# Kernel tuning notes

Measured on AMD Instinct MI355X. Metric: run time of the kernel, lower is better.

The kernel has to match this reference:

```python
import jax, jax.numpy as jnp
import numpy as np
from jax.ops import segment_sum

N = 100000
E = 2500000
F = 2
H = 32
L = 2


def setup_inputs() -> dict:
    key = jax.random.key(0)
    ks = jax.random.split(key, 12)
    s = 0.1
    node_features = jax.random.normal(ks[0], (N, F), dtype=jnp.float32)
    edge_index = jax.random.randint(ks[1], (2, E), 0, N, dtype=jnp.int64)
    W_in = jax.random.normal(ks[2], (F, H), dtype=jnp.float32) * s
    b_in = jnp.zeros((H,), dtype=jnp.float32)
    W_upd = jax.random.normal(ks[3], (L, 2 * H, H), dtype=jnp.float32) * s
    b_upd = jnp.zeros((L, H), dtype=jnp.float32)
    We1 = jax.random.normal(ks[4], (2 * H, H), dtype=jnp.float32) * s
    be1 = jnp.zeros((H,), dtype=jnp.float32)
    We2 = jax.random.normal(ks[5], (H, 1), dtype=jnp.float32) * s
    be2 = jnp.zeros((1,), dtype=jnp.float32)
    return {"node_features": node_features, "edge_index": edge_index,
            "W_in": W_in, "b_in": b_in, "W_upd": W_upd, "b_upd": b_upd,
            "We1": We1, "be1": be1, "We2": We2, "be2": be2}


def reference(node_features, edge_index, W_in, b_in, W_upd, b_upd, We1, be1, We2, be2):
    row, col = edge_index[0], edge_index[1]
    h = jax.nn.relu(node_features @ W_in + b_in)  # [N, H]
    # degree of each row node (bincount, clamped to >=1)
    deg = segment_sum(jnp.ones((E,), dtype=jnp.float32), row, num_segments=N)
    deg = jnp.maximum(deg, 1.0)[:, None]  # [N, 1]
    for l in range(L):
        agg = segment_sum(h[col], row, num_segments=N) / deg  # gather + scatter-add + normalize
        h = jax.nn.relu(jnp.concatenate([h, agg], axis=-1) @ W_upd[l] + b_upd[l])
    edge_feat = jnp.concatenate([h[row], h[col]], axis=-1)  # [E, 2H]
    hidden = jax.nn.relu(edge_feat @ We1 + be1)
    flux = (hidden @ We2 + be2)[:, 0]  # [E]
    return flux
```

## Files before the change

### kernel.cpp

```cpp
#include <hip/hip_runtime.h>
#include <hip/hip_fp16.h>

#define NN 100000
#define NE 2500000
#define RANGE 256
#define NBUCK 391
#define CHUNK 16384
#define NBLK_A ((NE + CHUNK - 1) / CHUNK)
#define BCAP 8192

__device__ __forceinline__ float relu_(float x){ return fmaxf(x, 0.f); }

__global__ __launch_bounds__(256) void k_node_embed16(
    const float* __restrict__ nf, const float* __restrict__ Win,
    const float* __restrict__ bin, __half* __restrict__ h16)
{
  int n = blockIdx.x * 256 + threadIdx.x;
  if (n >= NN) return;
  float f0 = nf[2*n], f1 = nf[2*n+1];
  const float4* W0 = (const float4*)Win;
  const float4* W1 = (const float4*)(Win + 32);
  const float4* B  = (const float4*)bin;
  __half2* g2 = (__half2*)(h16 + (size_t)n * 32);
#pragma unroll
  for (int j = 0; j < 8; ++j) {
    float4 w0 = W0[j], w1 = W1[j], b = B[j], r;
    r.x = relu_(fmaf(f0, w0.x, fmaf(f1, w1.x, b.x)));
    r.y = relu_(fmaf(f0, w0.y, fmaf(f1, w1.y, b.y)));
    r.z = relu_(fmaf(f0, w0.z, fmaf(f1, w1.z, b.z)));
    r.w = relu_(fmaf(f0, w0.w, fmaf(f1, w1.w, b.w)));
    g2[2*j]   = __floats2half2_rn(r.x, r.y);
    g2[2*j+1] = __floats2half2_rn(r.z, r.w);
  }
}


__global__ __launch_bounds__(512) void k_histA(const int* __restrict__ row,
                                               int* __restrict__ btot,
                                               int* __restrict__ blockhist)
{
  __shared__ int hist[NBUCK];
  int t = threadIdx.x;
  for (int i = t; i < NBUCK; i += 512) hist[i] = 0;
  __syncthreads();
  int e0 = blockIdx.x * CHUNK + t;
#pragma unroll
  for (int k = 0; k < CHUNK / 512; ++k) {
    int e = e0 + k * 512;
    if (e < NE) atomicAdd(&hist[row[e] >> 8], 1);
  }
  __syncthreads();
  for (int i = t; i < NBUCK; i += 512) {
    int c = hist[i];
    blockhist[(size_t)i * NBLK_A + blockIdx.x] = c;
    if (c) atomicAdd(&btot[i], c);
  }
}

__global__ __launch_bounds__(512) void k_scanA(const int* __restrict__ btot,
                                               int* __restrict__ bbase)
{
  __shared__ int s[512];
  int t = threadIdx.x;
  int my = (t < NBUCK) ? btot[t] : 0;
  s[t] = my;
  __syncthreads();
  for (int off = 1; off < 512; off <<= 1) {
    int v = (t >= off) ? s[t - off] : 0;
    __syncthreads();
    s[t] += v;
    __syncthreads();
  }
  if (t < NBUCK) bbase[t] = s[t] - my;
  if (t == 0) bbase[NBUCK] = NE;
}

__global__ __launch_bounds__(512) void k_colscan(int* __restrict__ blockhist,
                                                 const int* __restrict__ bbase)
{
  __shared__ int s[512];
  int i = blockIdx.x, t = threadIdx.x;
  int* rowp = blockhist + (size_t)i * NBLK_A;
  int my = (t < NBLK_A) ? rowp[t] : 0;
  s[t] = my;
  __syncthreads();
  for (int off = 1; off < 512; off <<= 1) {
    int v = (t >= off) ? s[t - off] : 0;
    __syncthreads();
    s[t] += v;
    __syncthreads();
  }
  if (t < NBLK_A) rowp[t] = bbase[i] + s[t] - my;
}

__global__ __launch_bounds__(512) void k_partition(
    const int* __restrict__ row, const int* __restrict__ col,
    const int* __restrict__ blockhist, unsigned int* __restrict__ keys)
{
  __shared__ int cur[NBUCK];
  __shared__ int base[NBUCK];
  int t = threadIdx.x, b = blockIdx.x;
  for (int i = t; i < NBUCK; i += 512) {
    base[i] = blockhist[(size_t)i * NBLK_A + b];
    cur[i] = 0;
  }
  __syncthreads();
  int e0 = b * CHUNK + t;
#pragma unroll
  for (int k = 0; k < CHUNK / 512; ++k) {
    int e = e0 + k * 512;
    if (e < NE) {
      int r = row[e];
      int bi = r >> 8;
      int idx = atomicAdd(&cur[bi], 1);
      keys[base[bi] + idx] = ((unsigned)col[e] << 8) | (unsigned)(r & 255);
    }
  }
}

__global__ __launch_bounds__(512) void k_passB_agg1(
    const int* __restrict__ bbase, const unsigned int* __restrict__ keys,
    const float* __restrict__ nf, const float* __restrict__ Win,
    const float* __restrict__ bin,
    int* __restrict__ ecol, int* __restrict__ rowptr,
    __half* __restrict__ agg16)
{
  __shared__ unsigned keysl[BCAP];
  __shared__ int hist[RANGE];
  __shared__ int sc[RANGE];
  __shared__ int segs[RANGE];
  __shared__ int sege[RANGE];
  int t = threadIdx.x, b = blockIdx.x;
  int s0 = bbase[b], e0 = bbase[b + 1];
  int cnt = e0 - s0;
  if (t < RANGE) hist[t] = 0;
  __syncthreads();
  for (int i = t; i < cnt; i += 512) {
    unsigned k = keys[s0 + i];
    if (i < BCAP) keysl[i] = k;
    atomicAdd(&hist[k & 255u], 1);
  }
  __syncthreads();
  int my = (t < RANGE) ? hist[t] : 0;
  if (t < RANGE) sc[t] = my;
  __syncthreads();
  for (int off = 1; off < RANGE; off <<= 1) {
    int v = 0;
    if (t < RANGE && t >= off) v = sc[t - off];
    __syncthreads();
    if (t < RANGE) sc[t] += v;
    __syncthreads();
  }
  if (t < RANGE) {
    int ex = sc[t] - my;
    int n = b * RANGE + t;
    if (n <= NN) rowptr[n] = s0 + ex;
    segs[t] = ex;
    sege[t] = sc[t];
    hist[t] = ex;
  }
  __syncthreads();
  for (int i = t; i < cnt; i += 512) {
    unsigned key = (i < BCAP) ? keysl[i] : keys[s0 + i];
    int rl = (int)(key & 255u);
    int idx = atomicAdd(&hist[rl], 1);
    ecol[s0 + idx] = (int)(key >> 8);
  }
  __syncthreads();

  const float2* nf2 = (const float2*)nf;
  for (int slot = t; slot < RANGE * 4; slot += 512) {
    int node = slot >> 2, q = slot & 3;
    int n = b * RANGE + node;
    if (n >= NN) continue;
    float w0[8], w1[8], bb[8];
#pragma unroll
    for (int j = 0; j < 8; ++j) {
      w0[j] = Win[q * 8 + j];
      w1[j] = Win[32 + q * 8 + j];
      bb[j] = bin[q * 8 + j];
    }
    int ss = segs[node], ee = sege[node];
    float acc[8];
#pragma unroll
    for (int j = 0; j < 8; ++j) acc[j] = 0.f;
    int i = ss;
    for (; i + 2 <= ee; i += 2) {
      int c0 = ecol[s0 + i], c1 = ecol[s0 + i + 1];
      float2 f0 = nf2[c0];
      float2 f1 = nf2[c1];
#pragma unroll
      for (int j = 0; j < 8; ++j) {
        acc[j] += relu_(fmaf(f0.x, w0[j], fmaf(f0.y, w1[j], bb[j])));
        acc[j] += relu_(fmaf(f1.x, w0[j], fmaf(f1.y, w1[j], bb[j])));
      }
    }
    if (i < ee) {
      float2 f = nf2[ecol[s0 + i]];
#pragma unroll
      for (int j = 0; j < 8; ++j)
        acc[j] += relu_(fmaf(f.x, w0[j], fmaf(f.y, w1[j], bb[j])));
    }
    float dinv = 1.0f / fmaxf((float)(ee - ss), 1.0f);
    uint4 pk;
    __half2* pp = (__half2*)&pk;
#pragma unroll
    for (int k = 0; k < 4; ++k)
      pp[k] = __floats2half2_rn(acc[2*k] * dinv, acc[2*k+1] * dinv);
    ((uint4*)agg16)[(size_t)n * 4 + q] = pk;
  }
}

__global__ __launch_bounds__(256) void k_update(
    const __half* __restrict__ h16in, const __half* __restrict__ agg16,
    const float* __restrict__ W, const float* __restrict__ b,
    __half* __restrict__ h16out)
{
  __shared__ float Ws[2048];
  __shared__ float bs[32];
  int t = threadIdx.x;
  for (int i = t; i < 2048; i += 256) Ws[i] = W[i];
  if (t < 32) bs[t] = b[t];
  __syncthreads();
  int n = blockIdx.x * 256 + t;
  if (n >= NN) return;

  float x[64];
  const uint4* hv = (const uint4*)(h16in + (size_t)n * 32);
  const uint4* av = (const uint4*)(agg16 + (size_t)n * 32);
#pragma unroll
  for (int j = 0; j < 4; ++j) {
    uint4 hx = hv[j], ax = av[j];
    const __half2* hp = (const __half2*)&hx;
    const __half2* ap = (const __half2*)&ax;
#pragma unroll
    for (int k = 0; k < 4; ++k) {
      float2 f = __half22float2(hp[k]);
      float2 g = __half22float2(ap[k]);
      x[j*8 + 2*k]      = f.x;
      x[j*8 + 2*k + 1]  = f.y;
      x[32 + j*8 + 2*k]     = g.x;
      x[32 + j*8 + 2*k + 1] = g.y;
    }
  }
  float acc[32];
#pragma unroll
  for (int j = 0; j < 32; ++j) acc[j] = bs[j];
#pragma unroll
  for (int k = 0; k < 64; ++k) {
    float xk = x[k];
    const float* wr = Ws + k * 32;
#pragma unroll
    for (int j = 0; j < 32; ++j) acc[j] = fmaf(xk, wr[j], acc[j]);
  }
  __half2* g2 = (__half2*)(h16out + (size_t)n * 32);
#pragma unroll
  for (int j = 0; j < 16; ++j)
    g2[j] = __floats2half2_rn(relu_(acc[2*j]), relu_(acc[2*j+1]));
}

__global__ __launch_bounds__(256) void k_agg_update2_uv(
    const int* __restrict__ rowptr, const int* __restrict__ ecol,
    const __half* __restrict__ h16in, const float* __restrict__ W,
    const float* __restrict__ b, const float* __restrict__ We1,
    const float* __restrict__ be1, __half* __restrict__ u,
    __half* __restrict__ v)
{
  __shared__ float Ws[2048];
  __shared__ float Es[2048];
  __shared__ float bs[32];
  __shared__ float bes[32];
  __shared__ float xs[64][65];
  int t = threadIdx.x;
  for (int i = t; i < 2048; i += 256) { Ws[i] = W[i]; Es[i] = We1[i]; }
  if (t < 32) { bs[t] = b[t]; bes[t] = be1[t]; }
  int q = t & 3, ln = t >> 2;
  int n = blockIdx.x * 64 + ln;
  bool act = (n < NN);
  const uint4* hv = (const uint4*)h16in;

  float acc[8];
#pragma unroll
  for (int j = 0; j < 8; ++j) acc[j] = 0.f;
  if (act) {
    int s = rowptr[n], e = rowptr[n + 1];
    int i = s;
    for (; i + 2 <= e; i += 2) {
      int c0 = ecol[i], c1 = ecol[i + 1];
      uint4 x0 = hv[c0 * 4 + q];
      uint4 x1 = hv[c1 * 4 + q];
      const __half2* p0 = (const __half2*)&x0;
      const __half2* p1 = (const __half2*)&x1;
#pragma unroll
      for (int k = 0; k < 4; ++k) {
        float2 f0 = __half22float2(p0[k]);
        float2 f1 = __half22float2(p1[k]);
        acc[2*k]   += f0.x + f1.x;
        acc[2*k+1] += f0.y + f1.y;
      }
    }
    if (i < e) {
      uint4 x = hv[ecol[i] * 4 + q];
      const __half2* hp = (const __half2*)&x;
#pragma unroll
      for (int k = 0; k < 4; ++k) {
        float2 f = __half22float2(hp[k]);
        acc[2*k] += f.x; acc[2*k+1] += f.y;
      }
    }
    float dinv = 1.0f / fmaxf((float)(e - s), 1.0f);
    uint4 hx = hv[n * 4 + q];
    const __half2* hp = (const __half2*)&hx;
#pragma unroll
    for (int k = 0; k < 4; ++k) {
      float2 f = __half22float2(hp[k]);
      xs[ln][q*8 + 2*k]     = f.x;
      xs[ln][q*8 + 2*k + 1] = f.y;
      xs[ln][32 + q*8 + 2*k]     = acc[2*k] * dinv;
      xs[ln][32 + q*8 + 2*k + 1] = acc[2*k+1] * dinv;
    }
  }
  __syncthreads();
  float h2[8];
#pragma unroll
  for (int j = 0; j < 8; ++j) h2[j] = bs[q*8 + j];
  if (act) {
    for (int k = 0; k < 64; ++k) {
      float xk = xs[ln][k];
      const float* wr = Ws + k * 32 + q * 8;
#pragma unroll
      for (int j = 0; j < 8; ++j) h2[j] = fmaf(xk, wr[j], h2[j]);
    }
#pragma unroll
    for (int j = 0; j < 8; ++j) h2[j] = relu_(h2[j]);
  }
  __syncthreads();
  if (act) {
#pragma unroll
    for (int j = 0; j < 8; ++j) xs[ln][q*8 + j] = h2[j];
  }
  __syncthreads();
  if (!act) return;
  float au[8], av[8];
#pragma unroll
  for (int j = 0; j < 8; ++j) { au[j] = bes[q*8 + j]; av[j] = 0.f; }
  for (int k = 0; k < 32; ++k) {
    float hk = xs[ln][k];
    const float* wu = Es + k * 32 + q * 8;
    const float* wv = Es + (32 + k) * 32 + q * 8;
#pragma unroll
    for (int j = 0; j < 8; ++j) {
      au[j] = fmaf(hk, wu[j], au[j]);
      av[j] = fmaf(hk, wv[j], av[j]);
    }
  }
  uint4 pu, pv;
  __half2* up = (__half2*)&pu;
  __half2* vp = (__half2*)&pv;
#pragma unroll
  for (int k = 0; k < 4; ++k) {
    up[k] = __floats2half2_rn(au[2*k], au[2*k+1]);
    vp[k] = __floats2half2_rn(av[2*k], av[2*k+1]);
  }
  ((uint4*)u)[n * 4 + q] = pu;
  ((uint4*)v)[n * 4 + q] = pv;
}

__global__ __launch_bounds__(256) void k_flux(
    const int* __restrict__ row, const int* __restrict__ col,
    const __half* __restrict__ u, const __half* __restrict__ v,
    const float* __restrict__ We2, const float* __restrict__ be2,
    float* __restrict__ out)
{
  int gid = blockIdx.x * 256 + threadIdx.x;
  int e = gid >> 2, q = gid & 3;
  if (e >= NE) return;
  int r = row[e], c = col[e];
  uint4 ua = ((const uint4*)u)[r * 4 + q];
  uint4 vb = ((const uint4*)v)[c * 4 + q];
  const __half2* ah = (const __half2*)&ua;
  const __half2* bh = (const __half2*)&vb;
  const float4* w4 = (const float4*)(We2 + q * 8);
  float4 w0 = w4[0], w1 = w4[1];
  float p = 0.f;
  {
    float2 a = __half22float2(ah[0]), b = __half22float2(bh[0]);
    p += relu_(a.x + b.x) * w0.x + relu_(a.y + b.y) * w0.y;
    a = __half22float2(ah[1]); b = __half22float2(bh[1]);
    p += relu_(a.x + b.x) * w0.z + relu_(a.y + b.y) * w0.w;
    a = __half22float2(ah[2]); b = __half22float2(bh[2]);
    p += relu_(a.x + b.x) * w1.x + relu_(a.y + b.y) * w1.y;
    a = __half22float2(ah[3]); b = __half22float2(bh[3]);
    p += relu_(a.x + b.x) * w1.z + relu_(a.y + b.y) * w1.w;
  }
  p += __shfl_xor(p, 1, 4);
  p += __shfl_xor(p, 2, 4);
  if (q == 0) out[e] = p + be2[0];
}

extern "C" void kernel_launch(void* const* d_in, const int* in_sizes, int n_in,
                              void* d_out, int out_size, void* d_ws, size_t ws_size,
                              hipStream_t stream) {
  const float* nf   = (const float*)d_in[0];
  const int*   ei   = (const int*)d_in[1];
  const float* Win  = (const float*)d_in[2];
  const float* bin  = (const float*)d_in[3];
  const float* Wupd = (const float*)d_in[4];
  const float* bupd = (const float*)d_in[5];
  const float* We1  = (const float*)d_in[6];
  const float* be1  = (const float*)d_in[7];
  const float* We2  = (const float*)d_in[8];
  const float* be2  = (const float*)d_in[9];
  float* out = (float*)d_out;

  const int* row = ei;
  const int* col = ei + NE;

  char* ws = (char*)d_ws;
  const size_t HB16 = (size_t)NN * 32 * 2;
  __half*       h16a  = (__half*)(ws);
  __half*       u     = (__half*)(ws);
  __half*       h16b  = (__half*)(ws + HB16);
  unsigned int* keys  = (unsigned int*)(ws + 2 * HB16);
  int*          ecol  = (int*)(ws + 2 * HB16 + 10000000);
  __half*       agg16 = (__half*)(ws + 2 * HB16 + 20000000);
  __half*       v     = (__half*)(ws + 2 * HB16 + 20000000 + HB16);
  char*         tail  = ws + 2 * HB16 + 20000000 + 2 * HB16;
  int*          rowptr    = (int*)(tail);
  int*          btot      = (int*)(tail + 400512);
  int*          bbase     = (int*)(tail + 402560);
  int*          blockhist = (int*)(tail + 404608);

  const int NB = (NN + 255) / 256;

  hipMemsetAsync(btot, 0, NBUCK * 4, stream);
  k_node_embed16<<<NB, 256, 0, stream>>>(nf, Win, bin, h16a);
  k_histA<<<NBLK_A, 512, 0, stream>>>(row, btot, blockhist);
  k_scanA<<<1, 512, 0, stream>>>(btot, bbase);
  k_colscan<<<NBUCK, 512, 0, stream>>>(blockhist, bbase);
  k_partition<<<NBLK_A, 512, 0, stream>>>(row, col, blockhist, keys);
  k_passB_agg1<<<NBUCK, 512, 0, stream>>>(bbase, keys, nf, Win, bin,
                                          ecol, rowptr, agg16);

  k_update<<<NB, 256, 0, stream>>>(h16a, agg16, Wupd, bupd, h16b);

  k_agg_update2_uv<<<(NN + 63) / 64, 256, 0, stream>>>(rowptr, ecol, h16b,
                                                       Wupd + 2048, bupd + 32,
                                                       We1, be1, u, v);

  k_flux<<<(NE * 4 + 255) / 256, 256, 0, stream>>>(row, col, u, v, We2, be2, out);
}
```

Before: 236.9 us.

## Fuse node embedding and layer-1 update into the bucketed aggregation kernel

Drops the separate node-embedding and layer-1 update kernels. The per-bucket aggregation kernel now recomputes the node's own embedding from the raw features, applies the 64x32 update matmul (spread across 4 lanes per node with shuffles) and writes h after layer 1 directly. This removes two launches and the round trips of h16a and agg16 through global memory. In exchange the aggregation kernel uses more shared memory and registers, which may lower occupancy in a kernel that runs only 391 blocks.

```diff
diff --git a/kernel.cpp b/kernel.cpp
--- a/kernel.cpp
+++ b/kernel.cpp
@@ -11,29 +11,6 @@
 
 __device__ __forceinline__ float relu_(float x){ return fmaxf(x, 0.f); }
 
-__global__ __launch_bounds__(256) void k_node_embed16(
-    const float* __restrict__ nf, const float* __restrict__ Win,
-    const float* __restrict__ bin, __half* __restrict__ h16)
-{
-  int n = blockIdx.x * 256 + threadIdx.x;
-  if (n >= NN) return;
-  float f0 = nf[2*n], f1 = nf[2*n+1];
-  const float4* W0 = (const float4*)Win;
-  const float4* W1 = (const float4*)(Win + 32);
-  const float4* B  = (const float4*)bin;
-  __half2* g2 = (__half2*)(h16 + (size_t)n * 32);
-#pragma unroll
-  for (int j = 0; j < 8; ++j) {
-    float4 w0 = W0[j], w1 = W1[j], b = B[j], r;
-    r.x = relu_(fmaf(f0, w0.x, fmaf(f1, w1.x, b.x)));
-    r.y = relu_(fmaf(f0, w0.y, fmaf(f1, w1.y, b.y)));
-    r.z = relu_(fmaf(f0, w0.z, fmaf(f1, w1.z, b.z)));
-    r.w = relu_(fmaf(f0, w0.w, fmaf(f1, w1.w, b.w)));
-    g2[2*j]   = __floats2half2_rn(r.x, r.y);
-    g2[2*j+1] = __floats2half2_rn(r.z, r.w);
-  }
-}
-
 
 __global__ __launch_bounds__(512) void k_histA(const int* __restrict__ row,
                                                int* __restrict__ btot,
@@ -118,19 +95,24 @@
   }
 }
 
-__global__ __launch_bounds__(512) void k_passB_agg1(
+__global__ __launch_bounds__(512) void k_passB_l1(
     const int* __restrict__ bbase, const unsigned int* __restrict__ keys,
     const float* __restrict__ nf, const float* __restrict__ Win,
-    const float* __restrict__ bin,
+    const float* __restrict__ bin, const float* __restrict__ W,
+    const float* __restrict__ bupd,
     int* __restrict__ ecol, int* __restrict__ rowptr,
-    __half* __restrict__ agg16)
+    __half* __restrict__ h16b)
 {
   __shared__ unsigned keysl[BCAP];
   __shared__ int hist[RANGE];
   __shared__ int sc[RANGE];
   __shared__ int segs[RANGE];
   __shared__ int sege[RANGE];
+  __shared__ float Ws[2048];
+  __shared__ float bs[32];
   int t = threadIdx.x, b = blockIdx.x;
+  for (int i = t; i < 2048; i += 512) Ws[i] = W[i];
+  if (t < 32) bs[t] = bupd[t];
   int s0 = bbase[b], e0 = bbase[b + 1];
   int cnt = e0 - s0;
   if (t < RANGE) hist[t] = 0;
@@ -202,61 +184,38 @@
         acc[j] += relu_(fmaf(f.x, w0[j], fmaf(f.y, w1[j], bb[j])));
     }
     float dinv = 1.0f / fmaxf((float)(ee - ss), 1.0f);
+    float g[8], a[8];
+    float2 fn = nf2[n];
+#pragma unroll
+    for (int j = 0; j < 8; ++j) {
+      g[j] = acc[j] * dinv;
+      a[j] = relu_(fmaf(fn.x, w0[j], fmaf(fn.y, w1[j], bb[j])));
+    }
+    float o[8];
+#pragma unroll
+    for (int j = 0; j < 8; ++j) o[j] = bs[q * 8 + j];
+#pragma unroll
+    for (int src = 0; src < 4; ++src) {
+#pragma unroll
+      for (int k = 0; k < 8; ++k) {
+        float xh = __shfl(a[k], src, 4);
+        float xg = __shfl(g[k], src, 4);
+        const float* wr1 = Ws + (src * 8 + k) * 32 + q * 8;
+        const float* wr2 = Ws + (32 + src * 8 + k) * 32 + q * 8;
+#pragma unroll
+        for (int j = 0; j < 8; ++j) {
+          o[j] = fmaf(xh, wr1[j], o[j]);
+          o[j] = fmaf(xg, wr2[j], o[j]);
+        }
+      }
+    }
     uint4 pk;
     __half2* pp = (__half2*)&pk;
 #pragma unroll
     for (int k = 0; k < 4; ++k)
-      pp[k] = __floats2half2_rn(acc[2*k] * dinv, acc[2*k+1] * dinv);
-    ((uint4*)agg16)[(size_t)n * 4 + q] = pk;
-  }
-}
-
-__global__ __launch_bounds__(256) void k_update(
-    const __half* __restrict__ h16in, const __half* __restrict__ agg16,
-    const float* __restrict__ W, const float* __restrict__ b,
-    __half* __restrict__ h16out)
-{
-  __shared__ float Ws[2048];
-  __shared__ float bs[32];
-  int t = threadIdx.x;
-  for (int i = t; i < 2048; i += 256) Ws[i] = W[i];
-  if (t < 32) bs[t] = b[t];
-  __syncthreads();
-  int n = blockIdx.x * 256 + t;
-  if (n >= NN) return;
-
-  float x[64];
-  const uint4* hv = (const uint4*)(h16in + (size_t)n * 32);
-  const uint4* av = (const uint4*)(agg16 + (size_t)n * 32);
-#pragma unroll
-  for (int j = 0; j < 4; ++j) {
-    uint4 hx = hv[j], ax = av[j];
-    const __half2* hp = (const __half2*)&hx;
-    const __half2* ap = (const __half2*)&ax;
-#pragma unroll
-    for (int k = 0; k < 4; ++k) {
-      float2 f = __half22float2(hp[k]);
-      float2 g = __half22float2(ap[k]);
-      x[j*8 + 2*k]      = f.x;
-      x[j*8 + 2*k + 1]  = f.y;
-      x[32 + j*8 + 2*k]     = g.x;
-      x[32 + j*8 + 2*k + 1] = g.y;
-    }
-  }
-  float acc[32];
-#pragma unroll
-  for (int j = 0; j < 32; ++j) acc[j] = bs[j];
-#pragma unroll
-  for (int k = 0; k < 64; ++k) {
-    float xk = x[k];
-    const float* wr = Ws + k * 32;
-#pragma unroll
-    for (int j = 0; j < 32; ++j) acc[j] = fmaf(xk, wr[j], acc[j]);
-  }
-  __half2* g2 = (__half2*)(h16out + (size_t)n * 32);
-#pragma unroll
-  for (int j = 0; j < 16; ++j)
-    g2[j] = __floats2half2_rn(relu_(acc[2*j]), relu_(acc[2*j+1]));
+      pp[k] = __floats2half2_rn(relu_(o[2*k]), relu_(o[2*k+1]));
+    ((uint4*)h16b)[(size_t)n * 4 + q] = pk;
+  }
 }
 
 __global__ __launch_bounds__(256) void k_agg_update2_uv(
@@ -418,31 +377,24 @@
 
   char* ws = (char*)d_ws;
   const size_t HB16 = (size_t)NN * 32 * 2;
-  __half*       h16a  = (__half*)(ws);
-  __half*       u     = (__half*)(ws);
-  __half*       h16b  = (__half*)(ws + HB16);
-  unsigned int* keys  = (unsigned int*)(ws + 2 * HB16);
-  int*          ecol  = (int*)(ws + 2 * HB16 + 10000000);
-  __half*       agg16 = (__half*)(ws + 2 * HB16 + 20000000);
-  __half*       v     = (__half*)(ws + 2 * HB16 + 20000000 + HB16);
-  char*         tail  = ws + 2 * HB16 + 20000000 + 2 * HB16;
+  unsigned int* keys = (unsigned int*)(ws);
+  int*          ecol = (int*)(ws + 10000000);
+  __half*       h16b = (__half*)(ws + 20000000);
+  __half*       u    = (__half*)(ws + 20000000 + HB16);
+  __half*       v    = (__half*)(ws + 20000000 + 2 * HB16);
+  char*         tail = ws + 20000000 + 3 * HB16;
   int*          rowptr    = (int*)(tail);
   int*          btot      = (int*)(tail + 400512);
   int*          bbase     = (int*)(tail + 402560);
   int*          blockhist = (int*)(tail + 404608);
 
-  const int NB = (NN + 255) / 256;
-
   hipMemsetAsync(btot, 0, NBUCK * 4, stream);
-  k_node_embed16<<<NB, 256, 0, stream>>>(nf, Win, bin, h16a);
   k_histA<<<NBLK_A, 512, 0, stream>>>(row, btot, blockhist);
   k_scanA<<<1, 512, 0, stream>>>(btot, bbase);
   k_colscan<<<NBUCK, 512, 0, stream>>>(blockhist, bbase);
   k_partition<<<NBLK_A, 512, 0, stream>>>(row, col, blockhist, keys);
-  k_passB_agg1<<<NBUCK, 512, 0, stream>>>(bbase, keys, nf, Win, bin,
-                                          ecol, rowptr, agg16);
-
-  k_update<<<NB, 256, 0, stream>>>(h16a, agg16, Wupd, bupd, h16b);
+  k_passB_l1<<<NBUCK, 512, 0, stream>>>(bbase, keys, nf, Win, bin,
+                                        Wupd, bupd, ecol, rowptr, h16b);
 
   k_agg_update2_uv<<<(NN + 63) / 64, 256, 0, stream>>>(rowptr, ecol, h16b,
                                                        Wupd + 2048, bupd + 32,
```

Measured after the change: 218.8 us. 7.6% less time.
